# Performance work log

Hardware: AMD Instinct MI355X
Metric: run time of the kernel (lower is better)

## Reference

```python
import jax, jax.numpy as jnp
import numpy as np

K = 7  # hardcoded pooling grid in the module


def setup_inputs() -> dict:
    key = jax.random.key(0)
    k1, k2, k3, k4, k5 = jax.random.split(key, 5)
    B, C1, H, W = 4, 21, 100, 100
    cls_conv_out = jax.random.normal(k1, (B, C1 * K * K, H, W), dtype=jnp.float32)
    n = 2000
    # ROIs: (ymin, xmin, ymax, xmax) integer coords; spans >= K so bin steps >= 1
    ymin = jax.random.randint(k2, (n,), 0, 40)
    ylen = jax.random.randint(k3, (n,), K, 57)
    xmin = jax.random.randint(k4, (n,), 0, 40)
    xlen = jax.random.randint(k5, (n,), K, 57)
    rois = jnp.stack([ymin, xmin, ymin + ylen, xmin + xlen], axis=1).astype(jnp.int32)
    return {"cls_conv_out": cls_conv_out, "rois": rois}


def _ps_roi_pool(cls_conv_out, rois):
    k = K
    B, C, H, W = cls_conv_out.shape
    c1 = C // (k * k)
    # Original indexes batch element `_ - 1` where `_` is the batch size -> last element.
    # Channel ordering from the `count` counter: channel = (j*k + l)*c1 + cls.
    feat = cls_conv_out[B - 1].reshape(k, k, c1, H, W)
    # Integral image (summed-area table) so each variable-size bin mean is 4 gathers.
    I = jnp.pad(feat, ((0, 0), (0, 0), (0, 0), (1, 0), (1, 0))).cumsum(axis=3).cumsum(axis=4)  # [k,k,c1,H+1,W+1]

    ymin, xmin, ymax, xmax = rois[:, 0], rois[:, 1], rois[:, 2], rois[:, 3]
    ys = (ymax - ymin) // k  # per-ROI bin step (int floor, as in int(range/k))
    xs = (xmax - xmin) // k
    j = jnp.arange(k)
    y0 = ymin[:, None] + j[None, :] * ys[:, None]  # [n,k] bin starts
    y1 = y0 + ys[:, None]                          # [n,k] bin stops
    x0 = xmin[:, None] + j[None, :] * xs[:, None]
    x1 = x0 + xs[:, None]

    jj = j[None, :, None, None]
    ll = j[None, None, :, None]
    cc = jnp.arange(c1)[None, None, None, :]
    Y0 = y0[:, :, None, None]; Y1 = y1[:, :, None, None]
    X0 = x0[:, None, :, None]; X1 = x1[:, None, :, None]
    # bin sums via SAT: [n, k, k, c1]
    S = (I[jj, ll, cc, Y1, X1] - I[jj, ll, cc, Y0, X1]
         - I[jj, ll, cc, Y1, X0] + I[jj, ll, cc,0*Y0 + Y0, X0])
    area = (ys * xs).astype(S.dtype)[:, None, None, None]
    pooled = S / area  # per-bin mean -> pooling_track, layout [n,k,k,c1]
    return pooled


def reference(cls_conv_out, rois):
    pooled = _ps_roi_pool(cls_conv_out, rois)          # [n,k,k,c1]
    avg = pooled.mean(axis=(1, 2))                     # AvgPool2d((7,7)) -> [n,c1]
    # nn.Softmax() on a 4D tensor applies over dim=1 (classes)
    scores = jax.nn.softmax(avg, axis=1)[:, :, None, None]  # [n,c1,1,1]
    return scores
```

## Files before the change

### kernel.cpp

```cpp
#include <hip/hip_runtime.h>
#include <math.h>

#define KK      7
#define C1      21
#define NPLANES (KK * KK * C1)
#define H       100
#define W       100
#define TS      101
#define NCHUNK  ((H * W) / 4)
#define PREFK   10

__global__ __launch_bounds__(256) void plane_partial(
    const float* __restrict__ src,
    size_t batch_off,
    const int*  __restrict__ rois,
    int nrois,
    float* __restrict__ partial)
{
    const int t  = threadIdx.x;
    const int p0 = blockIdx.x * 2;
    const int p1 = p0 + 1;
    const bool has_p1 = (p1 < NPLANES);

    __shared__ float tile[H * TS];

    {
        const float4* p4 = (const float4*)(src + batch_off + (size_t)p0 * (H * W));
        #pragma unroll
        for (int k = 0; k < PREFK; ++k) {
            int i = t + 256 * k;
            if (i < NCHUNK) {
                float4 v = p4[i];
                int g = i * 4;
                int y = g / W, x = g - y * W;
                float* d = &tile[y * TS + x];
                d[0] = v.x; d[1] = v.y; d[2] = v.z; d[3] = v.w;
            }
        }
    }
    __syncthreads();

    float4 pref[PREFK];
    if (has_p1) {
        const float4* p4 = (const float4*)(src + batch_off + (size_t)p1 * (H * W));
        #pragma unroll
        for (int k = 0; k < PREFK; ++k) {
            int i = t + 256 * k;
            if (i < NCHUNK) pref[k] = p4[i];
        }
    }

    for (int pass = 0; pass < 2; ++pass) {
        const int p = p0 + pass;
        if (p >= NPLANES) break;
        const int jl = p / C1;
        const int l  = jl % KK;
        const int j  = jl / KK;

        if (pass == 1) {
            __syncthreads();
            #pragma unroll
            for (int k = 0; k < PREFK; ++k) {
                int i = t + 256 * k;
                if (i < NCHUNK) {
                    float4 v = pref[k];
                    int g = i * 4;
                    int y = g / W, x = g - y * W;
                    float* d = &tile[y * TS + x];
                    d[0] = v.x; d[1] = v.y; d[2] = v.z; d[3] = v.w;
                }
            }
            __syncthreads();
        }

        if (t < H) {
            float s = 0.f;
            float* row = &tile[t * TS];
            for (int x = 0; x < W; ++x) { s += row[x]; row[x] = s; }
        }
        __syncthreads();

        if (t < W) {
            float s = 0.f;
            for (int y = 0; y < H; ++y) { s += tile[y * TS + t]; tile[y * TS + t] = s; }
        }
        __syncthreads();

        float* prow = partial + (size_t)p * nrois;
        for (int n = t; n < nrois; n += 256) {
            const int4 r  = ((const int4*)rois)[n];
            const int ys  = (r.z - r.x) / KK;
            const int xs  = (r.w - r.y) / KK;
            const int y0  = r.x + j * ys;
            const int x0  = r.y + l * xs;
            const int y1  = y0 + ys - 1;
            const int x1  = x0 + xs - 1;

            float S = tile[y1 * TS + x1];
            if (x0 > 0)           S -= tile[y1 * TS + (x0 - 1)];
            if (y0 > 0)           S -= tile[(y0 - 1) * TS + x1];
            if (y0 > 0 && x0 > 0) S += tile[(y0 - 1) * TS + (x0 - 1)];

            prow[n] = S;
        }
    }
}

#define RB 16

__global__ __launch_bounds__(256) void reduce_softmax(
    const float* __restrict__ partial,
    const int*   __restrict__ rois,
    int nrois,
    float*       __restrict__ out)
{
    const int dn = threadIdx.x & (RB - 1);
    const int cg = threadIdx.x / RB;
    const int n  = blockIdx.x * RB + dn;

    __shared__ float ch[RB][C1];

    if (n < nrois) {
        for (int c = cg; c < C1; c += 16) {
            float s = 0.f;
            const float* pc = partial + (size_t)c * nrois + n;
            #pragma unroll
            for (int jl = 0; jl < KK * KK; ++jl) {
                s += pc[(size_t)jl * C1 * nrois];
            }
            ch[dn][c] = s;
        }
    }
    __syncthreads();

    if (threadIdx.x < RB) {
        const int n2 = blockIdx.x * RB + threadIdx.x;
        if (n2 < nrois) {
            const int4 r  = ((const int4*)rois)[n2];
            const int ys  = (r.z - r.x) / KK;
            const int xs  = (r.w - r.y) / KK;
            const float inv = 1.0f / (49.0f * (float)(ys * xs));

            float v[C1];
            float m = -INFINITY;
            #pragma unroll
            for (int c = 0; c < C1; ++c) {
                v[c] = ch[threadIdx.x][c] * inv;
                m = fmaxf(m, v[c]);
            }
            float s = 0.f;
            #pragma unroll
            for (int c = 0; c < C1; ++c) { v[c] = __expf(v[c] - m); s += v[c]; }
            const float rs = 1.0f / s;
            #pragma unroll
            for (int c = 0; c < C1; ++c) out[(size_t)n2 * C1 + c] = v[c] * rs;
        }
    }
}

__global__ __launch_bounds__(256) void roi_pool_direct(
    const float* __restrict__ src,
    size_t batch_off,
    const int*   __restrict__ rois,
    float*       __restrict__ out)
{
    const int n = blockIdx.x;
    const int t = threadIdx.x;

    __shared__ float chsum[C1];
    if (t < C1) chsum[t] = 0.f;
    __syncthreads();

    const int ymin = rois[4 * n + 0];
    const int xmin = rois[4 * n + 1];
    const int ymax = rois[4 * n + 2];
    const int xmax = rois[4 * n + 3];
    const int ys = (ymax - ymin) / KK;
    const int xs = (xmax - xmin) / KK;

    const float* base = src + batch_off;

    for (int idx = t; idx < NPLANES; idx += blockDim.x) {
        const int c  = idx % C1;
        const int jl = idx / C1;
        const int l  = jl % KK;
        const int j  = jl / KK;
        const int y0 = ymin + j * ys;
        const int x0 = xmin + l * xs;
        const float* plane = base + (size_t)idx * (H * W);
        float s = 0.f;
        for (int y = y0; y < y0 + ys; ++y) {
            const float* row = plane + (size_t)y * W + x0;
            for (int x = 0; x < xs; ++x) s += row[x];
        }
        atomicAdd(&chsum[c], s);
    }
    __syncthreads();

    if (t == 0) {
        const float inv = 1.0f / (49.0f * (float)(ys * xs));
        float m = -INFINITY;
        float v[C1];
        for (int c = 0; c < C1; ++c) { v[c] = chsum[c] * inv; m = fmaxf(m, v[c]); }
        float s = 0.f;
        for (int c = 0; c < C1; ++c) { v[c] = expf(v[c] - m); s += v[c]; }
        const float rs = 1.0f / s;
        for (int c = 0; c < C1; ++c) out[(size_t)n * C1 + c] = v[c] * rs;
    }
}

extern "C" void kernel_launch(void* const* d_in, const int* in_sizes, int n_in,
                              void* d_out, int out_size, void* d_ws, size_t ws_size,
                              hipStream_t stream)
{
    const float* cls  = (const float*)d_in[0];
    const int*   rois = (const int*)d_in[1];
    float*       out  = (float*)d_out;

    const int nrois = in_sizes[1] / 4;
    const size_t plane_elems = (size_t)NPLANES * H * W;
    const int B = (int)((size_t)in_sizes[0] / plane_elems);
    const size_t batch_off = (size_t)(B - 1) * plane_elems;

    const size_t need = (size_t)NPLANES * nrois * sizeof(float);
    if (ws_size >= need) {
        float* partial = (float*)d_ws;
        const int nblocks = (NPLANES + 1) / 2;
        plane_partial<<<nblocks, 256, 0, stream>>>(cls, batch_off, rois, nrois, partial);
        reduce_softmax<<<(nrois + RB - 1) / RB, 256, 0, stream>>>(partial, rois, nrois, out);
    } else {
        roi_pool_direct<<<nrois, 256, 0, stream>>>(cls, batch_off, rois, out);
    }
}
```

Measured before the change: 213.8 us.

## Accumulate scaled bin sums atomically into output instead of partial buffer

```diff
diff --git a/kernel.cpp b/kernel.cpp
--- a/kernel.cpp
+++ b/kernel.cpp
@@ -9,13 +9,21 @@
 #define TS      101
 #define NCHUNK  ((H * W) / 4)
 #define PREFK   10
+#define SCHUNK  20
 
-__global__ __launch_bounds__(256) void plane_partial(
+
+__global__ __launch_bounds__(256) void zero_out(float* __restrict__ out, int n)
+{
+    int i = blockIdx.x * 256 + threadIdx.x;
+    if (i < n) out[i] = 0.0f;
+}
+
+__global__ __launch_bounds__(256) void plane_accum(
     const float* __restrict__ src,
     size_t batch_off,
     const int*  __restrict__ rois,
     int nrois,
-    float* __restrict__ partial)
+    float* __restrict__ acc)
 {
     const int t  = threadIdx.x;
     const int p0 = blockIdx.x * 2;
@@ -54,6 +62,7 @@
         const int p = p0 + pass;
         if (p >= NPLANES) break;
         const int jl = p / C1;
+        const int c  = p - jl * C1;
         const int l  = jl % KK;
         const int j  = jl / KK;
 
@@ -74,19 +83,30 @@
         }
 
         if (t < H) {
+            float* row = &tile[t * TS];
             float s = 0.f;
-            float* row = &tile[t * TS];
-            for (int x = 0; x < W; ++x) { s += row[x]; row[x] = s; }
+            for (int x0 = 0; x0 < W; x0 += SCHUNK) {
+                float v[SCHUNK];
+                #pragma unroll
+                for (int k = 0; k < SCHUNK; ++k) v[k] = row[x0 + k];
+                #pragma unroll
+                for (int k = 0; k < SCHUNK; ++k) { s += v[k]; row[x0 + k] = s; }
+            }
         }
         __syncthreads();
 
         if (t < W) {
             float s = 0.f;
-            for (int y = 0; y < H; ++y) { s += tile[y * TS + t]; tile[y * TS + t] = s; }
+            for (int y0 = 0; y0 < H; y0 += SCHUNK) {
+                float v[SCHUNK];
+                #pragma unroll
+                for (int k = 0; k < SCHUNK; ++k) v[k] = tile[(y0 + k) * TS + t];
+                #pragma unroll
+                for (int k = 0; k < SCHUNK; ++k) { s += v[k]; tile[(y0 + k) * TS + t] = s; }
+            }
         }
         __syncthreads();
 
-        float* prow = partial + (size_t)p * nrois;
         for (int n = t; n < nrois; n += 256) {
             const int4 r  = ((const int4*)rois)[n];
             const int ys  = (r.z - r.x) / KK;
@@ -101,112 +121,28 @@
             if (y0 > 0)           S -= tile[(y0 - 1) * TS + x1];
             if (y0 > 0 && x0 > 0) S += tile[(y0 - 1) * TS + (x0 - 1)];
 
-            prow[n] = S;
+            const float w = 1.0f / (49.0f * (float)(ys * xs));
+            atomicAdd(&acc[(size_t)n * C1 + c], S * w);
         }
     }
 }
 
-#define RB 16
+__global__ __launch_bounds__(64) void softmax_rows(float* __restrict__ outacc, int nrois)
+{
+    const int n = blockIdx.x * 64 + threadIdx.x;
+    if (n >= nrois) return;
+    float* row = outacc + (size_t)n * C1;
 
-__global__ __launch_bounds__(256) void reduce_softmax(
-    const float* __restrict__ partial,
-    const int*   __restrict__ rois,
-    int nrois,
-    float*       __restrict__ out)
-{
-    const int dn = threadIdx.x & (RB - 1);
-    const int cg = threadIdx.x / RB;
-    const int n  = blockIdx.x * RB + dn;
-
-    __shared__ float ch[RB][C1];
-
-    if (n < nrois) {
-        for (int c = cg; c < C1; c += 16) {
-            float s = 0.f;
-            const float* pc = partial + (size_t)c * nrois + n;
-            #pragma unroll
-            for (int jl = 0; jl < KK * KK; ++jl) {
-                s += pc[(size_t)jl * C1 * nrois];
-            }
-            ch[dn][c] = s;
-        }
-    }
-    __syncthreads();
-
-    if (threadIdx.x < RB) {
-        const int n2 = blockIdx.x * RB + threadIdx.x;
-        if (n2 < nrois) {
-            const int4 r  = ((const int4*)rois)[n2];
-            const int ys  = (r.z - r.x) / KK;
-            const int xs  = (r.w - r.y) / KK;
-            const float inv = 1.0f / (49.0f * (float)(ys * xs));
-
-            float v[C1];
-            float m = -INFINITY;
-            #pragma unroll
-            for (int c = 0; c < C1; ++c) {
-                v[c] = ch[threadIdx.x][c] * inv;
-                m = fmaxf(m, v[c]);
-            }
-            float s = 0.f;
-            #pragma unroll
-            for (int c = 0; c < C1; ++c) { v[c] = __expf(v[c] - m); s += v[c]; }
-            const float rs = 1.0f / s;
-            #pragma unroll
-            for (int c = 0; c < C1; ++c) out[(size_t)n2 * C1 + c] = v[c] * rs;
-        }
-    }
-}
-
-__global__ __launch_bounds__(256) void roi_pool_direct(
-    const float* __restrict__ src,
-    size_t batch_off,
-    const int*   __restrict__ rois,
-    float*       __restrict__ out)
-{
-    const int n = blockIdx.x;
-    const int t = threadIdx.x;
-
-    __shared__ float chsum[C1];
-    if (t < C1) chsum[t] = 0.f;
-    __syncthreads();
-
-    const int ymin = rois[4 * n + 0];
-    const int xmin = rois[4 * n + 1];
-    const int ymax = rois[4 * n + 2];
-    const int xmax = rois[4 * n + 3];
-    const int ys = (ymax - ymin) / KK;
-    const int xs = (xmax - xmin) / KK;
-
-    const float* base = src + batch_off;
-
-    for (int idx = t; idx < NPLANES; idx += blockDim.x) {
-        const int c  = idx % C1;
-        const int jl = idx / C1;
-        const int l  = jl % KK;
-        const int j  = jl / KK;
-        const int y0 = ymin + j * ys;
-        const int x0 = xmin + l * xs;
-        const float* plane = base + (size_t)idx * (H * W);
-        float s = 0.f;
-        for (int y = y0; y < y0 + ys; ++y) {
-            const float* row = plane + (size_t)y * W + x0;
-            for (int x = 0; x < xs; ++x) s += row[x];
-        }
-        atomicAdd(&chsum[c], s);
-    }
-    __syncthreads();
-
-    if (t == 0) {
-        const float inv = 1.0f / (49.0f * (float)(ys * xs));
-        float m = -INFINITY;
-        float v[C1];
-        for (int c = 0; c < C1; ++c) { v[c] = chsum[c] * inv; m = fmaxf(m, v[c]); }
-        float s = 0.f;
-        for (int c = 0; c < C1; ++c) { v[c] = expf(v[c] - m); s += v[c]; }
-        const float rs = 1.0f / s;
-        for (int c = 0; c < C1; ++c) out[(size_t)n * C1 + c] = v[c] * rs;
-    }
+    float v[C1];
+    float m = -INFINITY;
+    #pragma unroll
+    for (int c = 0; c < C1; ++c) { v[c] = row[c]; m = fmaxf(m, v[c]); }
+    float s = 0.f;
+    #pragma unroll
+    for (int c = 0; c < C1; ++c) { v[c] = __expf(v[c] - m); s += v[c]; }
+    const float rs = 1.0f / s;
+    #pragma unroll
+    for (int c = 0; c < C1; ++c) row[c] = v[c] * rs;
 }
 
 extern "C" void kernel_launch(void* const* d_in, const int* in_sizes, int n_in,
@@ -222,13 +158,11 @@
     const int B = (int)((size_t)in_sizes[0] / plane_elems);
     const size_t batch_off = (size_t)(B - 1) * plane_elems;
 
-    const size_t need = (size_t)NPLANES * nrois * sizeof(float);
-    if (ws_size >= need) {
-        float* partial = (float*)d_ws;
-        const int nblocks = (NPLANES + 1) / 2;
-        plane_partial<<<nblocks, 256, 0, stream>>>(cls, batch_off, rois, nrois, partial);
-        reduce_softmax<<<(nrois + RB - 1) / RB, 256, 0, stream>>>(partial, rois, nrois, out);
-    } else {
-        roi_pool_direct<<<nrois, 256, 0, stream>>>(cls, batch_off, rois, out);
-    }
+    const int ntot = nrois * C1;
+    zero_out<<<(ntot + 255) / 256, 256, 0, stream>>>(out, ntot);
+
+    const int nblocks = (NPLANES + 1) / 2;
+    plane_accum<<<nblocks, 256, 0, stream>>>(cls, batch_off, rois, nrois, out);
+
+    softmax_rows<<<(nrois + 63) / 64, 64, 0, stream>>>(out, nrois);
 }
```

New measurement: 313.0 us. 1.46x slower.
